# Kernel tuning notes

Hardware: AMD Instinct MI355X
Metric: run time of the kernel (lower is better)

The kernel has to match this reference:

```python
import jax, jax.numpy as jnp
import numpy as np

HIDDEN = 64
SEQ_LEN = 128
BATCH = 64
T_MAX = 20.0
BW = 1.0


def setup_inputs() -> dict:
    key = jax.random.key(0)
    ks = jax.random.split(key, 8)
    s = 1.0 / np.sqrt(HIDDEN)
    return {
        "rand_uniform_pool": jax.random.uniform(ks[0], (BATCH, SEQ_LEN), jnp.float32, 1e-6, 1.0),
        "expert_time": jax.random.uniform(ks[1], (BATCH, SEQ_LEN), jnp.float32, 0.0, 1.0),
        "W_ih": jax.random.uniform(ks[2], (4 * HIDDEN, 1), jnp.float32, -s, s),
        "W_hh": jax.random.uniform(ks[3], (4 * HIDDEN, HIDDEN), jnp.float32, -s, s),
        "b_ih": jax.random.uniform(ks[4], (4 * HIDDEN,), jnp.float32, -s, s),
        "b_hh": jax.random.uniform(ks[5], (4 * HIDDEN,), jnp.float32, -s, s),
        "V_w": jax.random.uniform(ks[6], (1, HIDDEN), jnp.float32, -s, s),
        "V_b": jax.random.uniform(ks[7], (1,), jnp.float32, -s, s),
    }


def _generate_time(rand_uniform_pool, W_ih, W_hh, b_ih, b_hh, V_w, V_b):
    # sequential rollout over SEQ_LEN steps (data-dependent recurrence)
    u_seq = rand_uniform_pool.T[:, :, None]  # [S, B, 1]

    def step(carry, u):
        hx, cx, cum = carry
        sigma = jax.nn.elu(hx @ V_w.T + V_b) + 1.0            # [B, 1]
        cum = cum + (-jnp.log(u)) / sigma                      # exponential inter-event time
        gates = cum @ W_ih.T + b_ih + hx @ W_hh.T + b_hh       # [B, 4H]
        i, f, g, o = jnp.split(gates, 4, axis=1)               # torch LSTMCell gate order
        cx = jax.nn.sigmoid(f) * cx + jax.nn.sigmoid(i) * jnp.tanh(g)
        hx = jax.nn.sigmoid(o) * jnp.tanh(cx)
        return (hx, cx, cum), cum[:, 0]

    init = (jnp.zeros((BATCH, HIDDEN), jnp.float32),
            jnp.zeros((BATCH, HIDDEN), jnp.float32),
            jnp.zeros((BATCH, 1), jnp.float32))
    _, cums = jax.lax.scan(step, init, u_seq)                  # [S, B]
    return cums.T                                              # [B, S]


def _reward(expert_time, learner_time):
    N = BATCH * SEQ_LEN
    t_l = learner_time.reshape(N)
    t_e = expert_time.reshape(N)
    m_l = ((t_l < T_MAX) & (t_l > 0)).astype(jnp.float32)
    m_e = ((t_e < T_MAX) & (t_e > 0)).astype(jnp.float32)

    def ksum(a, b, ma, mb):
        # ma^T exp(-(a-b)^2/bw) mb without storing more than one NxN matrix at a time
        K = jnp.exp(-((b[:, None] - a[None, :]) ** 2) / BW)    # [N, N]
        return jnp.dot(mb, K @ ma)

    ee = ksum(t_e, t_e, m_e, m_e)
    ll = ksum(t_l, t_l, m_l, m_l)
    le = ksum(t_l, t_e, m_l, m_e)
    return (ee + ll - 2.0 * le).reshape(1, 1)


def reference(rand_uniform_pool, expert_time, W_ih, W_hh, b_ih, b_hh, V_w, V_b):
    learner_time = _generate_time(rand_uniform_pool, W_ih, W_hh, b_ih, b_hh, V_w, V_b)
    loss = _reward(expert_time, learner_time)
    return loss
```

## Files before the change

### kernel.cpp

```cpp
#include <hip/hip_runtime.h>
#include <math.h>

#define HIDDEN 64
#define SEQ 128
#define BATCH 64
#define NPTS (BATCH * SEQ)
#define TMAXV 20.0f
#define L2E 1.4426950408889634f
#define LN2 0.6931471805599453f

typedef float v2f __attribute__((ext_vector_type(2)));

__device__ __forceinline__ float fexp2(float x) { return __builtin_amdgcn_exp2f(x); }
__device__ __forceinline__ float flog2(float x) { return __builtin_amdgcn_logf(x); }
__device__ __forceinline__ float frcp(float x)  { return __builtin_amdgcn_rcpf(x); }
__device__ __forceinline__ float fsigmoid(float x) { return frcp(1.0f + fexp2(-x * L2E)); }
__device__ __forceinline__ float ftanh(float x)    { return 1.0f - 2.0f * frcp(1.0f + fexp2(2.0f * x * L2E)); }

template <int CTRL>
__device__ __forceinline__ float dpp_mov(float x) {
    int r = __builtin_amdgcn_update_dpp(0, __float_as_int(x), CTRL, 0xf, 0xf, false);
    return __int_as_float(r);
}
__device__ __forceinline__ float wave_sum_dpp(float x) {
    x += dpp_mov<0x111>(x);
    x += dpp_mov<0x112>(x);
    x += dpp_mov<0x114>(x);
    x += dpp_mov<0x118>(x);
    x += dpp_mov<0x142>(x);
    x += dpp_mov<0x143>(x);
    return __int_as_float(__builtin_amdgcn_readlane(__float_as_int(x), 63));
}

__device__ __forceinline__ float wave_sum_shfl(float v) {
    v += __shfl_xor(v, 1);  v += __shfl_xor(v, 2);  v += __shfl_xor(v, 4);
    v += __shfl_xor(v, 8);  v += __shfl_xor(v, 16); v += __shfl_xor(v, 32);
    return v;
}

__global__ __launch_bounds__(256) void gen_and_ee(
    const float* __restrict__ upool,
    const float* __restrict__ texp,
    const float* __restrict__ Wih,
    const float* __restrict__ Whh,
    const float* __restrict__ bih,
    const float* __restrict__ bhh,
    const float* __restrict__ Vw,
    const float* __restrict__ Vb,
    float* __restrict__ tl,
    float* __restrict__ out)
{
    __shared__ float lu_s[SEQ];
    __shared__ float act_s[2][256];
    __shared__ __align__(16) float hx_s[4][64];
    __shared__ float2 qbuf[2048];

    const int bid = blockIdx.x;
    const int tid = threadIdx.x;

    if (bid < BATCH) {
        const int h  = tid & 63;
        const int wv = tid >> 6;

        v2f w2[32];
        const float4* wrow = (const float4*)(Whh + tid * 64);
        #pragma unroll
        for (int k = 0; k < 16; ++k) {
            float4 v = wrow[k];
            w2[2 * k]     = (v2f){v.x, v.y};
            w2[2 * k + 1] = (v2f){v.z, v.w};
        }
        const float bias = bih[tid] + bhh[tid];
        const float wih  = Wih[tid];
        const float vw   = Vw[h];
        const float vb   = Vb[0];

        if (tid < SEQ) lu_s[tid] = -flog2(upool[bid * SEQ + tid]) * LN2;
        hx_s[wv][h] = 0.0f;
        float cx = 0.0f;
        __syncthreads();

        float sg0 = (vb > 0.0f) ? (vb + 1.0f) : fexp2(vb * L2E);
        float cum = lu_s[0] * frcp(sg0);
        if (tid == 0) tl[bid * SEQ + 0] = cum;

        for (int s = 0; s < SEQ - 1; ++s) {
            const float4* h4 = (const float4*)hx_s[wv];
            v2f a0 = {0.f, 0.f}, a1 = {0.f, 0.f}, a2 = {0.f, 0.f}, a3 = {0.f, 0.f};
            #pragma unroll
            for (int k = 0; k < 16; k += 2) {
                float4 va = h4[k];
                float4 vbq = h4[k + 1];
                a0 = a0 + w2[2 * k]     * (v2f){va.x, va.y};
                a1 = a1 + w2[2 * k + 1] * (v2f){va.z, va.w};
                a2 = a2 + w2[2 * k + 2] * (v2f){vbq.x, vbq.y};
                a3 = a3 + w2[2 * k + 3] * (v2f){vbq.z, vbq.w};
            }
            v2f aa = (a0 + a1) + (a2 + a3);
            float g = (aa.x + aa.y) + bias + cum * wih;
            float a = (wv == 2) ? ftanh(g) : fsigmoid(g);
            act_s[s & 1][tid] = a;
            __syncthreads();

            float ig = act_s[s & 1][h];
            float fg = act_s[s & 1][64 + h];
            float gg = act_s[s & 1][128 + h];
            float og = act_s[s & 1][192 + h];
            cx = fg * cx + ig * gg;
            float hx = og * ftanh(cx);
            hx_s[wv][h] = hx;

            float tot = wave_sum_dpp(hx * vw);
            float xx  = tot + vb;
            float sg  = (xx > 0.0f) ? (xx + 1.0f) : fexp2(xx * L2E);
            cum += lu_s[s + 1] * frcp(sg);
            if (tid == 0) tl[bid * SEQ + s + 1] = cum;
        }
    } else {
        const int eb = bid - BATCH;
        const int pc = eb & 31;
        const int qs = eb >> 5;

        const int p = pc * 256 + tid;
        const float tp = texp[p];
        const float mp = (tp < TMAXV && tp > 0.0f) ? 1.0f : 0.0f;

        const int q0 = qs * 2048;
        for (int i = tid; i < 2048; i += 256) {
            float tq = texp[q0 + i];
            float mq = (tq < TMAXV && tq > 0.0f) ? 1.0f : 0.0f;
            qbuf[i] = make_float2(tq, mq);
        }
        __syncthreads();

        float acc = 0.0f;
        #pragma unroll 4
        for (int i = 0; i < 2048; ++i) {
            float2 qq = qbuf[i];
            float d = tp - qq.x;
            acc = fmaf(qq.y, fexp2(d * d * (-L2E)), acc);
        }
        acc *= mp;
        acc = wave_sum_shfl(acc);
        if ((tid & 63) == 0) atomicAdd(out, acc);
    }
}

__global__ __launch_bounds__(256) void ll_le(
    const float* __restrict__ texp,
    const float* __restrict__ tl,
    float* __restrict__ out)
{
    __shared__ __align__(16) float4 qbuf[512];
    __shared__ float red[4];

    const int pc = blockIdx.x;
    const int qs = blockIdx.y;
    const int tid = threadIdx.x;

    const int p = pc * 256 + tid;
    const float tlp = tl[p];
    const float mlp = (tlp < TMAXV && tlp > 0.0f) ? 1.0f : 0.0f;

    const int q0 = qs * 512;
    for (int i = tid; i < 512; i += 256) {
        float tq = tl[q0 + i];
        float mq = (tq < TMAXV && tq > 0.0f) ? 1.0f : 0.0f;
        float te = texp[q0 + i];
        float me = (te < TMAXV && te > 0.0f) ? 1.0f : 0.0f;
        qbuf[i] = make_float4(tq, mq, te, me);
    }
    __syncthreads();

    float val = 0.0f;
    if (__ballot(mlp != 0.0f) != 0ULL) {
        float a_ll = 0.0f, a_le = 0.0f;
        #pragma unroll 4
        for (int i = 0; i < 512; ++i) {
            float4 q = qbuf[i];
            float d1 = tlp - q.x;
            a_ll = fmaf(q.y, fexp2(d1 * d1 * (-L2E)), a_ll);
            float d2 = tlp - q.z;
            a_le = fmaf(q.w, fexp2(d2 * d2 * (-L2E)), a_le);
        }
        val = mlp * (a_ll - 2.0f * a_le);
    }

    val = wave_sum_shfl(val);
    if ((tid & 63) == 0) red[tid >> 6] = val;
    __syncthreads();
    if (tid == 0) atomicAdd(out, red[0] + red[1] + red[2] + red[3]);
}

extern "C" void kernel_launch(void* const* d_in, const int* in_sizes, int n_in,
                              void* d_out, int out_size, void* d_ws, size_t ws_size,
                              hipStream_t stream) {
    const float* upool = (const float*)d_in[0];
    const float* texp  = (const float*)d_in[1];
    const float* Wih   = (const float*)d_in[2];
    const float* Whh   = (const float*)d_in[3];
    const float* bih   = (const float*)d_in[4];
    const float* bhh   = (const float*)d_in[5];
    const float* Vw    = (const float*)d_in[6];
    const float* Vb    = (const float*)d_in[7];
    float* out = (float*)d_out;
    float* tl  = (float*)d_ws;

    hipMemsetAsync(out, 0, sizeof(float), stream);
    hipLaunchKernelGGL(gen_and_ee, dim3(BATCH + 128), dim3(256), 0, stream,
                       upool, texp, Wih, Whh, bih, bhh, Vw, Vb, tl, out);
    hipLaunchKernelGGL(ll_le, dim3(32, 16), dim3(256), 0, stream, texp, tl, out);
}
```

Measured before the change: 160.8 us.

## Run LSTM recurrence in a single wave with all four gates per thread

```diff
diff --git a/kernel.cpp b/kernel.cpp
--- a/kernel.cpp
+++ b/kernel.cpp
@@ -38,7 +38,7 @@
     return v;
 }
 
-__global__ __launch_bounds__(256) void gen_and_ee(
+__global__ __launch_bounds__(256, 1) void gen_and_ee(
     const float* __restrict__ upool,
     const float* __restrict__ texp,
     const float* __restrict__ Wih,
@@ -51,71 +51,97 @@
     float* __restrict__ out)
 {
     __shared__ float lu_s[SEQ];
-    __shared__ float act_s[2][256];
-    __shared__ __align__(16) float hx_s[4][64];
+    __shared__ __align__(16) float hx_s[HIDDEN];
     __shared__ float2 qbuf[2048];
 
     const int bid = blockIdx.x;
     const int tid = threadIdx.x;
 
     if (bid < BATCH) {
-        const int h  = tid & 63;
-        const int wv = tid >> 6;
-
-        v2f w2[32];
-        const float4* wrow = (const float4*)(Whh + tid * 64);
-        #pragma unroll
-        for (int k = 0; k < 16; ++k) {
-            float4 v = wrow[k];
-            w2[2 * k]     = (v2f){v.x, v.y};
-            w2[2 * k + 1] = (v2f){v.z, v.w};
-        }
-        const float bias = bih[tid] + bhh[tid];
-        const float wih  = Wih[tid];
-        const float vw   = Vw[h];
-        const float vb   = Vb[0];
-
-        if (tid < SEQ) lu_s[tid] = -flog2(upool[bid * SEQ + tid]) * LN2;
-        hx_s[wv][h] = 0.0f;
+        if (tid >= 64) return;
+        const int h = tid;
+
+        v2f wi[32], wf[32], wg[32], wo[32];
+        {
+            const float4* r0 = (const float4*)(Whh + (h) * HIDDEN);
+            const float4* r1 = (const float4*)(Whh + (64 + h) * HIDDEN);
+            const float4* r2 = (const float4*)(Whh + (128 + h) * HIDDEN);
+            const float4* r3 = (const float4*)(Whh + (192 + h) * HIDDEN);
+            #pragma unroll
+            for (int k = 0; k < 16; ++k) {
+                float4 v0 = r0[k]; wi[2*k] = (v2f){v0.x, v0.y}; wi[2*k+1] = (v2f){v0.z, v0.w};
+                float4 v1 = r1[k]; wf[2*k] = (v2f){v1.x, v1.y}; wf[2*k+1] = (v2f){v1.z, v1.w};
+                float4 v2_ = r2[k]; wg[2*k] = (v2f){v2_.x, v2_.y}; wg[2*k+1] = (v2f){v2_.z, v2_.w};
+                float4 v3 = r3[k]; wo[2*k] = (v2f){v3.x, v3.y}; wo[2*k+1] = (v2f){v3.z, v3.w};
+            }
+        }
+        const float bi_ = bih[h]        + bhh[h];
+        const float bf_ = bih[64 + h]   + bhh[64 + h];
+        const float bg_ = bih[128 + h]  + bhh[128 + h];
+        const float bo_ = bih[192 + h]  + bhh[192 + h];
+        const float wii = Wih[h], wif = Wih[64 + h], wig = Wih[128 + h], wio = Wih[192 + h];
+        const float vw = Vw[h];
+        const float vb = Vb[0];
+
+        lu_s[h]      = -flog2(upool[bid * SEQ + h]) * LN2;
+        lu_s[64 + h] = -flog2(upool[bid * SEQ + 64 + h]) * LN2;
+        hx_s[h] = 0.0f;
         float cx = 0.0f;
-        __syncthreads();
 
         float sg0 = (vb > 0.0f) ? (vb + 1.0f) : fexp2(vb * L2E);
         float cum = lu_s[0] * frcp(sg0);
-        if (tid == 0) tl[bid * SEQ + 0] = cum;
-
+        float keep0 = (h == 0) ? cum : 0.0f;
+        float keep1 = 0.0f;
+
+        #pragma unroll 1
         for (int s = 0; s < SEQ - 1; ++s) {
-            const float4* h4 = (const float4*)hx_s[wv];
-            v2f a0 = {0.f, 0.f}, a1 = {0.f, 0.f}, a2 = {0.f, 0.f}, a3 = {0.f, 0.f};
+            float lunext = lu_s[s + 1];
+            const float4* h4 = (const float4*)hx_s;
+            v2f i0={0.f,0.f}, i1={0.f,0.f}, i2={0.f,0.f}, i3={0.f,0.f};
+            v2f f0={0.f,0.f}, f1={0.f,0.f}, f2={0.f,0.f}, f3={0.f,0.f};
+            v2f g0={0.f,0.f}, g1={0.f,0.f}, g2={0.f,0.f}, g3={0.f,0.f};
+            v2f o0={0.f,0.f}, o1={0.f,0.f}, o2={0.f,0.f}, o3={0.f,0.f};
             #pragma unroll
             for (int k = 0; k < 16; k += 2) {
-                float4 va = h4[k];
-                float4 vbq = h4[k + 1];
-                a0 = a0 + w2[2 * k]     * (v2f){va.x, va.y};
-                a1 = a1 + w2[2 * k + 1] * (v2f){va.z, va.w};
-                a2 = a2 + w2[2 * k + 2] * (v2f){vbq.x, vbq.y};
-                a3 = a3 + w2[2 * k + 3] * (v2f){vbq.z, vbq.w};
+                float4 va4 = h4[k];
+                float4 vb4 = h4[k + 1];
+                v2f x0 = (v2f){va4.x, va4.y};
+                v2f x1 = (v2f){va4.z, va4.w};
+                v2f x2 = (v2f){vb4.x, vb4.y};
+                v2f x3 = (v2f){vb4.z, vb4.w};
+                i0 += wi[2*k] * x0; i1 += wi[2*k+1] * x1; i2 += wi[2*k+2] * x2; i3 += wi[2*k+3] * x3;
+                f0 += wf[2*k] * x0; f1 += wf[2*k+1] * x1; f2 += wf[2*k+2] * x2; f3 += wf[2*k+3] * x3;
+                g0 += wg[2*k] * x0; g1 += wg[2*k+1] * x1; g2 += wg[2*k+2] * x2; g3 += wg[2*k+3] * x3;
+                o0 += wo[2*k] * x0; o1 += wo[2*k+1] * x1; o2 += wo[2*k+2] * x2; o3 += wo[2*k+3] * x3;
             }
-            v2f aa = (a0 + a1) + (a2 + a3);
-            float g = (aa.x + aa.y) + bias + cum * wih;
-            float a = (wv == 2) ? ftanh(g) : fsigmoid(g);
-            act_s[s & 1][tid] = a;
-            __syncthreads();
-
-            float ig = act_s[s & 1][h];
-            float fg = act_s[s & 1][64 + h];
-            float gg = act_s[s & 1][128 + h];
-            float og = act_s[s & 1][192 + h];
-            cx = fg * cx + ig * gg;
+            v2f ia = (i0 + i1) + (i2 + i3);
+            v2f fa = (f0 + f1) + (f2 + f3);
+            v2f ga = (g0 + g1) + (g2 + g3);
+            v2f oa = (o0 + o1) + (o2 + o3);
+            float gi = (ia.x + ia.y) + bi_ + cum * wii;
+            float gf = (fa.x + fa.y) + bf_ + cum * wif;
+            float gg = (ga.x + ga.y) + bg_ + cum * wig;
+            float go = (oa.x + oa.y) + bo_ + cum * wio;
+
+            float ig = fsigmoid(gi);
+            float fg = fsigmoid(gf);
+            float gt = ftanh(gg);
+            float og = fsigmoid(go);
+            cx = fg * cx + ig * gt;
             float hx = og * ftanh(cx);
-            hx_s[wv][h] = hx;
+            hx_s[h] = hx;
 
             float tot = wave_sum_dpp(hx * vw);
             float xx  = tot + vb;
             float sg  = (xx > 0.0f) ? (xx + 1.0f) : fexp2(xx * L2E);
-            cum += lu_s[s + 1] * frcp(sg);
-            if (tid == 0) tl[bid * SEQ + s + 1] = cum;
-        }
+            cum += lunext * frcp(sg);
+
+            const int sp = s + 1;
+            keep0 = (h == sp) ? cum : keep0;
+            keep1 = (h == sp - 64) ? cum : keep1;
+        }
+        tl[bid * SEQ + h]      = keep0;
+        tl[bid * SEQ + 64 + h] = keep1;
     } else {
         const int eb = bid - BATCH;
         const int pc = eb & 31;
```

After: 214.0 us. 33.1% more time.
